# Performance work log

Measured on AMD Instinct MI355X. Metric: run time of the kernel, lower is better.

The kernel has to match this reference:

```python
import jax, jax.numpy as jnp
import numpy as np

SEQ, BSZ = 512, 128
VOC, EMB, HDIM = 50000, 128, 256
TAGS = 7
BOS, EOS, PAD = 4, 5, 6
H = HDIM // 2  # per-direction hidden size
NEG = -10000.0


def setup_inputs() -> dict:
    key = jax.random.key(0)
    ks = jax.random.split(key, 12)
    s = 0.08  # ~ pytorch default init scale for these sizes
    trans = jax.random.normal(ks[10], (TAGS, TAGS), dtype=jnp.float32)
    # constraints applied in __init__: no transition FROM BOS targets / INTO EOS etc.
    trans = trans.at[BOS, :].set(NEG).at[:, EOS].set(NEG).at[PAD, :].set(0.0)
    return {
        "sen": jax.random.randint(ks[0], (SEQ, BSZ), 0, VOC),                # (S, B) token ids
        "emb": jax.random.normal(ks[1], (VOC, EMB), jnp.float32) * s,        # embedding table
        "Wih_f": jax.random.normal(ks[2], (4 * H, EMB), jnp.float32) * s,    # fwd dir, gates i,f,g,o
        "Whh_f": jax.random.normal(ks[3], (4 * H, H), jnp.float32) * s,
        "b_f": jax.random.normal(ks[4], (4 * H,), jnp.float32) * s,          # b_ih + b_hh fused
        "Wih_b": jax.random.normal(ks[5], (4 * H, EMB), jnp.float32) * s,    # bwd dir
        "Whh_b": jax.random.normal(ks[6], (4 * H, H), jnp.float32) * s,
        "b_b": jax.random.normal(ks[7], (4 * H,), jnp.float32) * s,
        "W_out": jax.random.normal(ks[8], (TAGS, HDIM), jnp.float32) * s,    # hid2tag
        "b_out": jax.random.normal(ks[9], (TAGS,), jnp.float32) * s,
        "trans": trans,                                                      # trans[next, prev]
    }


def _lstm_dir(x, Wih, Whh, b, reverse):
    """Single-direction LSTM over (S, B, E) -> (S, B, H). PyTorch gate order i,f,g,o."""
    xw = jnp.einsum('sbe,ge->sbg', x, Wih) + b  # hoist input projection out of scan

    def step(carry, xt):
        h, c = carry
        g = xt + h @ Whh.T
        i, f, gg, o = jnp.split(g, 4, axis=-1)
        c = jax.nn.sigmoid(f) * c + jax.nn.sigmoid(i) * jnp.tanh(gg)
        h = jax.nn.sigmoid(o) * jnp.tanh(c)
        return (h, c), h

    B = x.shape[1]
    h0 = jnp.zeros((B, H), x.dtype)
    _, hs = jax.lax.scan(step, (h0, h0), xw, reverse=reverse)
    return hs


def reference(sen, emb, Wih_f, Whh_f, b_f, Wih_b, Whh_b, b_b, W_out, b_out, trans):
    # ----- BiLSTM features -----
    x = emb[sen]                                   # (S, B, E)
    hf = _lstm_dir(x, Wih_f, Whh_f, b_f, reverse=False)
    hb = _lstm_dir(x, Wih_b, Whh_b, b_b, reverse=True)
    fts = jnp.concatenate([hf, hb], axis=-1) @ W_out.T + b_out   # (S, B, TAGS)

    # ----- Viterbi decode (batched, one scan over sequence) -----
    B = fts.shape[1]
    fv0 = jnp.full((B, TAGS), NEG, dtype=fts.dtype).at[:, BOS].set(0.0)

    def vstep(fv, ft):
        # scores[b, next, prev] = fv[b, prev] + trans[next, prev]
        scores = fv[:, None, :] + trans[None, :, :]
        bptr = jnp.argmax(scores, axis=2)          # (B, TAGS) best prev per next tag
        fv_new = jnp.max(scores, axis=2) + ft
        return fv_new, bptr

    fv, bptrs = jax.lax.scan(vstep, fv0, fts)      # bptrs: (S, B, TAGS)
    terminal = fv + trans[EOS]                     # (B, TAGS)
    best = jnp.argmax(terminal, axis=1)            # (B,)
    path_score = jnp.take_along_axis(terminal, best[:, None], axis=1)[:, 0]

    def bstep(cur, bptr):
        prev = jnp.take_along_axis(bptr, cur[:, None], axis=1)[:, 0]
        return prev, cur                           # output = tag at this position

    _, tag_seq = jax.lax.scan(bstep, best, bptrs, reverse=True)  # (S, B)
    return path_score, tag_seq
```

## Files before the change

### kernel.cpp

```cpp
#include <hip/hip_runtime.h>
#include <hip/hip_bf16.h>
#include <math.h>

#define SEQ  512
#define BSZ  128
#define EMBD 128
#define H4   512
#define HD   128
#define NTAG 7
#define BOSX 4
#define EOSX 5
#define NEGC (-10000.0f)

typedef _Float16 h2 __attribute__((ext_vector_type(2)));
typedef _Float16 f16x8 __attribute__((ext_vector_type(8)));
typedef float    f32x4 __attribute__((ext_vector_type(4)));

__device__ __forceinline__ float frcp(float x) { return __builtin_amdgcn_rcpf(x); }

template<int C> __device__ __forceinline__ float dppmovf(float x) {
    return __builtin_bit_cast(float,
        __builtin_amdgcn_update_dpp(0, __builtin_bit_cast(int, x), C, 0xF, 0xF, true));
}
template<int C> __device__ __forceinline__ int dppmovi(int x) {
    return __builtin_amdgcn_update_dpp(0, x, C, 0xF, 0xF, true);
}

__global__ __launch_bounds__(512) __attribute__((amdgpu_waves_per_eu(1, 2)))
void bilstm_fused(const int* __restrict__ sen, const float* __restrict__ emb,
                  const float* __restrict__ Wih_f, const float* __restrict__ b_f,
                  const float* __restrict__ Wih_b, const float* __restrict__ b_b,
                  const float* __restrict__ Whh_f, const float* __restrict__ Whh_b,
                  const float* __restrict__ W_out,
                  float* __restrict__ eft, float* __restrict__ ebt)
{
    const int tid = threadIdx.x;
    const int wid = tid >> 6;
    const int lane = tid & 63;
    const int col = lane & 15;
    const int kg  = lane >> 4;
    const bool bk0 = (lane & 1) != 0;
    const bool bk1 = (lane & 2) != 0;
    const int chain = blockIdx.x;
    const int dir = chain & 1;
    const int b = chain >> 1;
    const int t0 = dir ? (SEQ - 1) : 0;
    const int ts = dir ? -1 : 1;

    __shared__ __align__(16) _Float16 xA[2][4][4][16][8];
    __shared__ __align__(16) float zb[2][8][512];
    __shared__ __align__(16) _Float16 hA[2][128];

    const float* __restrict__ Wih  = dir ? Wih_b : Wih_f;
    const float* __restrict__ Whh  = dir ? Whh_b : Whh_f;
    const float* __restrict__ bias = dir ? b_b  : b_f;

    f16x8 bw[4][4], bwh[4][4], be[4];
    float biasv[4];
    #pragma unroll
    for (int tt = 0; tt < 4; ++tt) {
        const int R = (wid * 4 + tt) * 16 + col;
        const int ug = R >> 2;
        const int gg = R & 3;
        #pragma unroll
        for (int ks = 0; ks < 4; ++ks) {
            const float* s1 = Wih + (gg * HD + ug) * EMBD + ks * 32 + kg * 8;
            const float* s2 = Whh + (gg * HD + ug) * HD   + ks * 32 + kg * 8;
            f16x8 v1, v2;
            #pragma unroll
            for (int j = 0; j < 8; ++j) { v1[j] = (_Float16)s1[j]; v2[j] = (_Float16)s2[j]; }
            bw[tt][ks] = v1; bwh[tt][ks] = v2;
        }
        biasv[tt] = bias[gg * HD + ug];
    }
    #pragma unroll
    for (int ks = 0; ks < 4; ++ks) {
        f16x8 v;
        #pragma unroll
        for (int j = 0; j < 8; ++j)
            v[j] = (col < NTAG) ? (_Float16)W_out[col * 256 + dir * HD + ks * 32 + kg * 8 + j]
                                : (_Float16)0.f;
        be[ks] = v;
    }

    if (tid < 256) ((_Float16*)hA)[tid] = (_Float16)0.f;
    {
        unsigned* p = (unsigned*)xA;
        p[tid] = 0u; p[tid + 512] = 0u; p[tid + 1024] = 0u; p[tid + 1536] = 0u;
    }

    const int srow = wid;
    const int sp = lane;
    float2 sv;
    auto sissue = [&](int w) {
        const int row = w * 8 + srow;
        const int tg = t0 + ts * row;
        const int tok = sen[tg * BSZ + b];
        sv = *(const float2*)(emb + (size_t)tok * EMBD + 2 * sp);
    };
    auto swrite = [&](int buf) {
        h2 t; t.x = (_Float16)sv.x; t.y = (_Float16)sv.y;
        *(unsigned*)&xA[buf][sp >> 4][(sp >> 2) & 3][srow][(sp & 3) * 2]
            = __builtin_bit_cast(unsigned, t);
    };

    auto proj = [&](int bufp, int nb) {
        f16x8 ax[4];
        #pragma unroll
        for (int ks = 0; ks < 4; ++ks)
            ax[ks] = *(const f16x8*)&xA[bufp][ks][kg][col][0];
        f32x4 acc[4];
        #pragma unroll
        for (int tt = 0; tt < 4; ++tt) { acc[tt][0]=0.f; acc[tt][1]=0.f; acc[tt][2]=0.f; acc[tt][3]=0.f; }
        #pragma unroll
        for (int ks = 0; ks < 4; ++ks)
            #pragma unroll
            for (int tt = 0; tt < 4; ++tt)
                acc[tt] = __builtin_amdgcn_mfma_f32_16x16x32_f16(ax[ks], bw[tt][ks], acc[tt], 0, 0, 0);
        if (lane < 32) {
            #pragma unroll
            for (int tt = 0; tt < 4; ++tt)
                #pragma unroll
                for (int r = 0; r < 4; ++r)
                    zb[nb][(lane >> 4) * 4 + r][wid * 64 + tt * 16 + col]
                        = acc[tt][r] + biasv[tt];
        }
    };

    float c = 0.0f;
    float* __restrict__ eX = (dir ? ebt : eft) + (size_t)b * (SEQ * 8);

    sissue(0); swrite(0);
    sissue(1); swrite(1);
    __syncthreads();
    proj(0, 0);
    sissue(2);
    __syncthreads();

    for (int base = 0; base < SEQ; base += 8) {
        const int W = base >> 3;
        #pragma unroll
        for (int sl = 0; sl < 8; ++sl) {
            const int s = base + sl;
            const int cur = sl & 1;
            f16x8 ah[4];
            #pragma unroll
            for (int ks = 0; ks < 4; ++ks)
                ah[ks] = *(const f16x8*)&hA[cur][ks * 32 + kg * 8];
            if (sl == 0) {
                if (base <= SEQ - 24) swrite(W & 1);
                if (base <= SEQ - 32) sissue(W + 3);
                if (W < 63) proj((W & 1) ^ 1, (W & 1) ^ 1);
            }
            f32x4 acc[4];
            #pragma unroll
            for (int tt = 0; tt < 4; ++tt) { acc[tt][0]=0.f; acc[tt][1]=0.f; acc[tt][2]=0.f; acc[tt][3]=0.f; }
            #pragma unroll
            for (int ks = 0; ks < 4; ++ks)
                #pragma unroll
                for (int tt = 0; tt < 4; ++tt)
                    acc[tt] = __builtin_amdgcn_mfma_f32_16x16x32_f16(ah[ks], bwh[tt][ks], acc[tt], 0, 0, 0);
            f32x4 eacc; eacc[0]=0.f; eacc[1]=0.f; eacc[2]=0.f; eacc[3]=0.f;
            if (wid == 7 && s >= 1) {
                #pragma unroll
                for (int ks = 0; ks < 4; ++ks)
                    eacc = __builtin_amdgcn_mfma_f32_16x16x32_f16(ah[ks], be[ks], eacc, 0, 0, 0);
            }
            const bool isg = bk1 && !bk0;
            float y[4];
            #pragma unroll
            for (int tt = 0; tt < 4; ++tt) {
                const float z = acc[tt][0] + zb[W & 1][sl][wid * 64 + tt * 16 + col];
                const float x2 = isg ? (z + z) : z;
                const float yy = frcp(1.0f + __expf(-x2));
                y[tt] = isg ? (2.0f * yy - 1.0f) : yy;
            }
            const float n0 = bk0 ? dppmovf<0xB1>(y[1]) : y[0];
            const float n1 = bk0 ? y[1] : dppmovf<0xB1>(y[0]);
            const float n2 = bk0 ? dppmovf<0xB1>(y[3]) : y[2];
            const float n3 = bk0 ? y[3] : dppmovf<0xB1>(y[2]);
            const float m0 = bk1 ? dppmovf<0x4E>(n2) : n0;
            const float m2 = bk1 ? n2 : dppmovf<0x4E>(n0);
            const float m1 = bk1 ? dppmovf<0x4E>(n3) : n1;
            const float m3 = bk1 ? n3 : dppmovf<0x4E>(n1);
            c = m1 * c + m0 * m2;
            const float th = 2.0f * frcp(1.0f + __expf(-2.0f * c)) - 1.0f;
            const float h = m3 * th;
            if (kg == 0)
                hA[cur ^ 1][wid * 16 + (lane & 3) * 4 + (lane >> 2)] = (_Float16)h;
            if (wid == 7 && s >= 1 && kg == 0 && col < NTAG)
                eX[(t0 + ts * (s - 1)) * 8 + col] = eacc[0];
            __syncthreads();
        }
    }

    if (wid == 7) {
        f16x8 ah[4];
        #pragma unroll
        for (int ks = 0; ks < 4; ++ks)
            ah[ks] = *(const f16x8*)&hA[0][ks * 32 + kg * 8];
        f32x4 eacc; eacc[0]=0.f; eacc[1]=0.f; eacc[2]=0.f; eacc[3]=0.f;
        #pragma unroll
        for (int ks = 0; ks < 4; ++ks)
            eacc = __builtin_amdgcn_mfma_f32_16x16x32_f16(ah[ks], be[ks], eacc, 0, 0, 0);
        if (kg == 0 && col < NTAG)
            eX[(t0 + ts * (SEQ - 1)) * 8 + col] = eacc[0];
    }
}

__global__ __launch_bounds__(256, 1)
void vit_kernel(const float* __restrict__ eft, const float* __restrict__ ebt,
                const float* __restrict__ b_out, const float* __restrict__ trans,
                float* __restrict__ out)
{
    const int b = blockIdx.x;
    const int tid = threadIdx.x;
    __shared__ __align__(16) float ftl[SEQ * 8];
    __shared__ unsigned wordL[SEQ];

    {
        const float4* sf = (const float4*)(eft + (size_t)b * (SEQ * 8));
        const float4* sb = (const float4*)(ebt + (size_t)b * (SEQ * 8));
        float4* dst = (float4*)ftl;
        #pragma unroll
        for (int i = 0; i < SEQ * 2 / 256; ++i) {
            const int idx = tid + i * 256;
            float4 a = sf[idx];
            const float4 c4 = sb[idx];
            a.x += c4.x; a.y += c4.y; a.z += c4.z; a.w += c4.w;
            dst[idx] = a;
        }
    }
    __syncthreads();

    if (tid < 64) {
        const int lane = tid;
        const int next = lane >> 3;
        const int prev = lane & 7;
        const bool pv = (prev < NTAG);
        const bool nv = (next < NTAG);
        const float trv = (pv && nv) ? (trans[next * NTAG + prev] + b_out[next]) : -3.0e38f;
        float fvp = pv ? ((prev == BOSX) ? 0.0f : NEGC) : -3.0e38f;

        for (int t = 0; t < SEQ; ++t) {
            float mv = fvp + trv;
            int am = prev;
            {
                const float om = dppmovf<0xB1>(mv); const int oa = dppmovi<0xB1>(am);
                if (om > mv || (om == mv && oa < am)) { mv = om; am = oa; }
            }
            {
                const float om = dppmovf<0x4E>(mv); const int oa = dppmovi<0x4E>(am);
                if (om > mv || (om == mv && oa < am)) { mv = om; am = oa; }
            }
            {
                const float om = dppmovf<0x141>(mv); const int oa = dppmovi<0x141>(am);
                if (om > mv || (om == mv && oa < am)) { mv = om; am = oa; }
            }
            const float fvnew = mv + ftl[t * 8 + next];
            const float nfv = __shfl(fvnew, (lane & 7) << 3);
            const int   amg = __shfl(am,    (lane & 7) << 3);
            unsigned pw = (unsigned)amg << (3 * prev);
            pw |= (unsigned)dppmovi<0xB1>((int)pw);
            pw |= (unsigned)dppmovi<0x4E>((int)pw);
            pw |= (unsigned)dppmovi<0x141>((int)pw);
            if (lane == 0) wordL[t] = pw;
            fvp = pv ? nfv : -3.0e38f;
        }

        float term = pv ? (fvp + trans[EOSX * NTAG + prev]) : -3.0e38f;
        int am = prev;
        {
            const float om = dppmovf<0xB1>(term); const int oa = dppmovi<0xB1>(am);
            if (om > term || (om == term && oa < am)) { term = om; am = oa; }
        }
        {
            const float om = dppmovf<0x4E>(term); const int oa = dppmovi<0x4E>(am);
            if (om > term || (om == term && oa < am)) { term = om; am = oa; }
        }
        {
            const float om = dppmovf<0x141>(term); const int oa = dppmovi<0x141>(am);
            if (om > term || (om == term && oa < am)) { term = om; am = oa; }
        }
        if (lane == 0) out[b] = term;

        unsigned wd[8];
        #pragma unroll
        for (int c2 = 0; c2 < 8; ++c2) wd[c2] = wordL[c2 * 64 + lane];
        int cur = __builtin_amdgcn_readfirstlane(am);
        unsigned pr[8];
        #pragma unroll
        for (int c2 = 7; c2 >= 0; --c2) {
            unsigned acc = 0u;
            for (int tt = 63; tt >= 0; --tt) {
                acc = (lane == tt) ? (unsigned)cur : acc;
                const unsigned w = (unsigned)__builtin_amdgcn_readlane((int)wd[c2], tt);
                cur = (int)((w >> (3 * cur)) & 7u);
            }
            pr[c2] = acc;
        }
        #pragma unroll
        for (int c2 = 0; c2 < 8; ++c2)
            out[BSZ + (c2 * 64 + lane) * BSZ + b] = (float)pr[c2];
    }
}

extern "C" void kernel_launch(void* const* d_in, const int* in_sizes, int n_in,
                              void* d_out, int out_size, void* d_ws, size_t ws_size,
                              hipStream_t stream)
{
    const int*   sen   = (const int*)d_in[0];
    const float* emb   = (const float*)d_in[1];
    const float* Wih_f = (const float*)d_in[2];
    const float* Whh_f = (const float*)d_in[3];
    const float* b_f   = (const float*)d_in[4];
    const float* Wih_b = (const float*)d_in[5];
    const float* Whh_b = (const float*)d_in[6];
    const float* b_b   = (const float*)d_in[7];
    const float* W_out = (const float*)d_in[8];
    const float* b_out = (const float*)d_in[9];
    const float* trans = (const float*)d_in[10];
    float* out = (float*)d_out;

    char* ws = (char*)d_ws;
    const size_t ft_bytes = (size_t)BSZ * SEQ * 8 * 4;
    float* eft = (float*)ws;
    float* ebt = (float*)(ws + ft_bytes);

    bilstm_fused<<<dim3(2 * BSZ), dim3(512), 0, stream>>>(
        sen, emb, Wih_f, b_f, Wih_b, b_b, Whh_f, Whh_b, W_out, eft, ebt);
    vit_kernel<<<dim3(BSZ), dim3(256), 0, stream>>>(eft, ebt, b_out, trans, out);
}
```

Measured before the change: 597.4 us.

## Split recurrent MFMA chains, prefetch next-step gate bias, batch emission stores

The serial recurrent h@Whh product is split into two independent accumulator chains so the dependent MFMA latency is shortened. The precomputed input-projection value for the next step is loaded from LDS into registers one step ahead. Emission outputs are buffered in registers and written every 8 steps instead of every step. __syncthreads is replaced by a custom barrier that waits only on LDS counters, which avoids waiting on global stores. The costs are more registers and reliance on correct waitcnt semantics for the global stores that are no longer covered by the barrier.

```diff
diff --git a/kernel.cpp b/kernel.cpp
--- a/kernel.cpp
+++ b/kernel.cpp
@@ -24,6 +24,13 @@
 }
 template<int C> __device__ __forceinline__ int dppmovi(int x) {
     return __builtin_amdgcn_update_dpp(0, x, C, 0xF, 0xF, true);
+}
+
+__device__ __forceinline__ void step_barrier() {
+    __builtin_amdgcn_sched_barrier(0);
+    asm volatile("s_waitcnt lgkmcnt(0)" ::: "memory");
+    __builtin_amdgcn_s_barrier();
+    __builtin_amdgcn_sched_barrier(0);
 }
 
 __global__ __launch_bounds__(512) __attribute__((amdgpu_waves_per_eu(1, 2)))
@@ -128,6 +135,8 @@
     };
 
     float c = 0.0f;
+    float ebuf[8];
+    float zqA[4], zqB[4];
     float* __restrict__ eX = (dir ? ebt : eft) + (size_t)b * (SEQ * 8);
 
     sissue(0); swrite(0);
@@ -136,6 +145,9 @@
     proj(0, 0);
     sissue(2);
     __syncthreads();
+    #pragma unroll
+    for (int tt = 0; tt < 4; ++tt)
+        zqA[tt] = zb[0][0][wid * 64 + tt * 16 + col];
 
     for (int base = 0; base < SEQ; base += 8) {
         const int W = base >> 3;
@@ -143,6 +155,8 @@
         for (int sl = 0; sl < 8; ++sl) {
             const int s = base + sl;
             const int cur = sl & 1;
+            float* zc = (sl & 1) ? zqB : zqA;
+            float* zo = (sl & 1) ? zqA : zqB;
             f16x8 ah[4];
             #pragma unroll
             for (int ks = 0; ks < 4; ++ks)
@@ -152,25 +166,38 @@
                 if (base <= SEQ - 32) sissue(W + 3);
                 if (W < 63) proj((W & 1) ^ 1, (W & 1) ^ 1);
             }
-            f32x4 acc[4];
-            #pragma unroll
-            for (int tt = 0; tt < 4; ++tt) { acc[tt][0]=0.f; acc[tt][1]=0.f; acc[tt][2]=0.f; acc[tt][3]=0.f; }
-            #pragma unroll
-            for (int ks = 0; ks < 4; ++ks)
-                #pragma unroll
-                for (int tt = 0; tt < 4; ++tt)
-                    acc[tt] = __builtin_amdgcn_mfma_f32_16x16x32_f16(ah[ks], bwh[tt][ks], acc[tt], 0, 0, 0);
-            f32x4 eacc; eacc[0]=0.f; eacc[1]=0.f; eacc[2]=0.f; eacc[3]=0.f;
+            f32x4 accA[4], accB[4];
+            #pragma unroll
+            for (int tt = 0; tt < 4; ++tt) {
+                accA[tt][0]=0.f; accA[tt][1]=0.f; accA[tt][2]=0.f; accA[tt][3]=0.f;
+                accB[tt][0]=0.f; accB[tt][1]=0.f; accB[tt][2]=0.f; accB[tt][3]=0.f;
+            }
+            #pragma unroll
+            for (int tt = 0; tt < 4; ++tt) {
+                accA[tt] = __builtin_amdgcn_mfma_f32_16x16x32_f16(ah[0], bwh[tt][0], accA[tt], 0, 0, 0);
+                accB[tt] = __builtin_amdgcn_mfma_f32_16x16x32_f16(ah[2], bwh[tt][2], accB[tt], 0, 0, 0);
+                accA[tt] = __builtin_amdgcn_mfma_f32_16x16x32_f16(ah[1], bwh[tt][1], accA[tt], 0, 0, 0);
+                accB[tt] = __builtin_amdgcn_mfma_f32_16x16x32_f16(ah[3], bwh[tt][3], accB[tt], 0, 0, 0);
+            }
             if (wid == 7 && s >= 1) {
+                f32x4 eacc; eacc[0]=0.f; eacc[1]=0.f; eacc[2]=0.f; eacc[3]=0.f;
                 #pragma unroll
                 for (int ks = 0; ks < 4; ++ks)
                     eacc = __builtin_amdgcn_mfma_f32_16x16x32_f16(ah[ks], be[ks], eacc, 0, 0, 0);
+                ebuf[sl] = eacc[0];
+            }
+            if (s + 1 < SEQ) {
+                const int nbuf = (sl == 7) ? ((W & 1) ^ 1) : (W & 1);
+                const int nsl = (sl + 1) & 7;
+                #pragma unroll
+                for (int tt = 0; tt < 4; ++tt)
+                    zo[tt] = zb[nbuf][nsl][wid * 64 + tt * 16 + col];
             }
             const bool isg = bk1 && !bk0;
             float y[4];
             #pragma unroll
             for (int tt = 0; tt < 4; ++tt) {
-                const float z = acc[tt][0] + zb[W & 1][sl][wid * 64 + tt * 16 + col];
+                const float z = accA[tt][0] + accB[tt][0] + zc[tt];
                 const float x2 = isg ? (z + z) : z;
                 const float yy = frcp(1.0f + __expf(-x2));
                 y[tt] = isg ? (2.0f * yy - 1.0f) : yy;
@@ -188,9 +215,14 @@
             const float h = m3 * th;
             if (kg == 0)
                 hA[cur ^ 1][wid * 16 + (lane & 3) * 4 + (lane >> 2)] = (_Float16)h;
-            if (wid == 7 && s >= 1 && kg == 0 && col < NTAG)
-                eX[(t0 + ts * (s - 1)) * 8 + col] = eacc[0];
-            __syncthreads();
+            if (sl == 7 && wid == 7 && kg == 0 && col < NTAG) {
+                #pragma unroll
+                for (int r = 0; r < 8; ++r) {
+                    const int e = base - 1 + r;
+                    if (e >= 0) eX[(t0 + ts * e) * 8 + col] = ebuf[r];
+                }
+            }
+            step_barrier();
         }
     }
 
```

After: 592.8 us. No clear change (-0.8%).
